# Kernel optimization log

Measured on AMD Instinct MI355X. Metric: run time of the kernel, lower is better.

The kernel has to match this reference:

```python
import jax, jax.numpy as jnp
import numpy as np

B, T, C = 4, 2048, 1024
NH, HS = 16, 64            # n_head, head_size
BL, SL = 32, 16            # block_length, stride_length


def setup_inputs() -> dict:
    key = jax.random.key(0)
    ks = jax.random.split(key, 7)
    def lin(k, shape, fan_in):
        return jax.random.normal(k, shape, jnp.float32) * (1.0 / np.sqrt(fan_in))
    return {
        "x": jax.random.normal(ks[0], (B, T, C), jnp.float32),
        "W_attn": lin(ks[1], (3 * C, C), C),          # c_attn weight (bias=False)
        "W_proj": lin(ks[2], (C, C), C),              # c_proj weight
        "pos_emb": jax.random.normal(ks[3], (T, HS), jnp.float32) * 0.02,
        "W_fc": lin(ks[4], (4 * HS, BL * HS), BL * HS),   # compression c_fc
        "W_cproj": lin(ks[5], (HS, 4 * HS), 4 * HS),      # compression c_proj
        "ln_w": jnp.ones((HS,), jnp.float32),             # compression LayerNorm (bias=False)
    }


def _compress(h, pos_emb, W_fc, W_cproj, ln_w):
    # h: [B, nh, T, hs] -> [B, nh, num_blocks, hs] ; sliding windows of len BL, stride SL
    Bb, nh, Tt, hs = h.shape
    nb = max(1, (Tt - BL) // SL + 1)
    idx = jnp.arange(nb)[:, None] * SL + jnp.arange(BL)[None, :]        # [nb, BL]
    blocks = h[:, :, idx, :] + pos_emb[:BL][None, None, None, :, :]     # [B,nh,nb,BL,hs]
    flat = blocks.reshape(Bb, nh, nb, BL * hs)
    z = jax.nn.gelu(jnp.einsum('bnkf,gf->bnkg', flat, W_fc), approximate=False)
    z = jnp.einsum('bnkg,hg->bnkh', z, W_cproj)
    mu = jnp.mean(z, axis=-1, keepdims=True)
    var = jnp.var(z, axis=-1, keepdims=True)
    return (z - mu) / jnp.sqrt(var + 1e-5) * ln_w


def reference(x, W_attn, W_proj, pos_emb, W_fc, W_cproj, ln_w):
    Bb, Tt, Cc = x.shape
    qkv = x @ W_attn.T                                   # [B,T,3C]
    q, k, v = jnp.split(qkv, 3, axis=-1)
    q = q.reshape(Bb, Tt, NH, HS).transpose(0, 2, 1, 3)  # [B,nh,T,hs]
    k = k.reshape(Bb, Tt, NH, HS).transpose(0, 2, 1, 3)
    v = v.reshape(Bb, Tt, NH, HS).transpose(0, 2, 1, 3)

    # Computed (and discarded) exactly as in the torch forward.
    _kc = _compress(k, pos_emb, W_fc, W_cproj, ln_w)
    _vc = _compress(v, pos_emb, W_fc, W_cproj, ln_w)

    # Flash branch: is_causal=True -> attn_mask=None -> plain causal SDPA
    scale = 1.0 / np.sqrt(HS)
    scores = jnp.einsum('bhqd,bhkd->bhqk', q, k) * scale          # [B,nh,T,T]
    causal = jnp.tril(jnp.ones((Tt, Tt), dtype=bool))
    scores = jnp.where(causal, scores, -jnp.inf)
    att = jax.nn.softmax(scores, axis=-1)
    y = jnp.einsum('bhqk,bhkd->bhqd', att, v)                     # [B,nh,T,hs]
    y = y.transpose(0, 2, 1, 3).reshape(Bb, Tt, Cc)
    return y @ W_proj.T
```

## Files before the change

### kernel.cpp

```cpp
#include <hip/hip_runtime.h>
#include <hip/hip_bf16.h>
#include <stdint.h>


typedef __bf16 bf16x8 __attribute__((ext_vector_type(8)));
typedef float f32x4 __attribute__((ext_vector_type(4)));
typedef __hip_bfloat16 bf16;

#define B_ 4
#define T_ 2048
#define C_ 1024
#define NH_ 16
#define HS_ 64
#define NEG_BIG (-30000.0f)
#define SCALE_LOG2E 0.180336880111f

__device__ __forceinline__ bool detect_fp32(const unsigned short* px) {
  const int lane = threadIdx.x & 63;
  const unsigned short u = px[2 * lane];
  const int e = (u >> 7) & 0xff;
  const bool plausible = (e >= 117) && (e <= 137);
  return __popcll(__ballot(plausible)) < 32;
}

__device__ __forceinline__ void load_lds16(const bf16* g, bf16* l) {
  __builtin_amdgcn_global_load_lds(
      (const __attribute__((address_space(1))) void*)(uintptr_t)g,
      (__attribute__((address_space(3))) void*)(uintptr_t)l, 16, 0, 0);
}

__device__ __forceinline__ uint4 ld8f(const void* base, size_t elt) {
  const float* fp = (const float*)base + elt;
  float4 f0 = *(const float4*)(fp);
  float4 f1 = *(const float4*)(fp + 4);
  union { bf16 h[8]; uint4 u; } r;
  r.h[0] = __float2bfloat16(f0.x); r.h[1] = __float2bfloat16(f0.y);
  r.h[2] = __float2bfloat16(f0.z); r.h[3] = __float2bfloat16(f0.w);
  r.h[4] = __float2bfloat16(f1.x); r.h[5] = __float2bfloat16(f1.y);
  r.h[6] = __float2bfloat16(f1.z); r.h[7] = __float2bfloat16(f1.w);
  return r.u;
}

__global__ __launch_bounds__(256) void convert3(
    const void* __restrict__ x, const void* __restrict__ wa,
    const void* __restrict__ wp, bf16* __restrict__ xb, bf16* __restrict__ wab,
    bf16* __restrict__ wpb, const unsigned short* __restrict__ probe) {
  const bool f32 = detect_fp32(probe);
  int blk = blockIdx.x;
  const void* src;
  bf16* dst;
  if (blk < 4096) {
    src = x; dst = xb;
  } else if (blk < 4096 + 1536) {
    blk -= 4096; src = wa; dst = wab;
  } else {
    blk -= 4096 + 1536; src = wp; dst = wpb;
  }
  const size_t i = ((size_t)blk * 256 + threadIdx.x) * 8;
  if (f32)
    *(uint4*)(dst + i) = ld8f(src, i);
  else
    *(uint4*)(dst + i) = *(const uint4*)((const bf16*)src + i);
}

template <int IN_MODE, int OUT_MODE>
__global__ __launch_bounds__(256, 2) void gemm_bt(
    const void* __restrict__ A, const void* __restrict__ B, void* __restrict__ C,
    bf16* __restrict__ k_ws, bf16* __restrict__ v_ws,
    const unsigned short* __restrict__ in_probe,
    const unsigned short* __restrict__ out_probe, int M, int N, int K) {
  __shared__ bf16 As[128 * 32];
  __shared__ bf16 Bs[128 * 32];

  const bool f32b = in_probe ? detect_fp32(in_probe) : false;
  const bool f32a = (IN_MODE == 0) && f32b;
  const bool f32out =
      (OUT_MODE == 0) && (out_probe ? detect_fp32(out_probe) : false);

  const int tid = threadIdx.x;
  const int lane = tid & 63;
  const int wid = tid >> 6;
  const int quad = lane >> 4;
  const int col = lane & 15;
  const int m0 = blockIdx.y * 128;
  const int n0 = blockIdx.x * 128;
  const int wm = (wid >> 1) * 64;
  const int wn = (wid & 1) * 64;
  const bool vsec = (OUT_MODE == 1) && ((n0 >> 10) == 2);

  const size_t arow = (size_t)(m0 + (tid >> 2));
  const size_t brow = (size_t)(n0 + (tid >> 2));
  const int chunk = (tid & 3) * 8;

  f32x4 acc[4][4] = {};

  for (int k0 = 0; k0 < K; k0 += 32) {
    const bf16* ap0;
    const bf16* ap1;
    if (IN_MODE == 0) {
      ap0 = (const bf16*)A + arow * K + chunk + k0;
      ap1 = (const bf16*)A + (arow + 64) * K + chunk + k0;
    } else {
      const int b = m0 >> 11;
      const int tloc = (m0 & 2047) + (tid >> 2);
      const size_t aoff = ((((size_t)b * NH_) + (k0 >> 6)) * T_ + tloc) * HS_ +
                          (k0 & 32) + chunk;
      ap0 = (const bf16*)A + aoff;
      ap1 = (const bf16*)A + aoff + (size_t)64 * HS_;
    }

    uint4 a0, a1, b0, b1;
    if (f32a) {
      a0 = ld8f(A, arow * K + chunk + k0);
      a1 = ld8f(A, (arow + 64) * K + chunk + k0);
    }
    if (f32b) {
      b0 = ld8f(B, brow * K + chunk + k0);
      b1 = ld8f(B, (brow + 64) * K + chunk + k0);
    }

    __syncthreads();
    if (f32a) {
      *(uint4*)(As + tid * 8) = a0;
      *(uint4*)(As + 2048 + tid * 8) = a1;
    } else {
      load_lds16(ap0, As + tid * 8);
      load_lds16(ap1, As + 2048 + tid * 8);
    }
    if (f32b) {
      *(uint4*)(Bs + tid * 8) = b0;
      *(uint4*)(Bs + 2048 + tid * 8) = b1;
    } else {
      load_lds16((const bf16*)B + brow * K + chunk + k0, Bs + tid * 8);
      load_lds16((const bf16*)B + (brow + 64) * K + chunk + k0,
                 Bs + 2048 + tid * 8);
    }
    __syncthreads();

    bf16x8 af[4], bfr[4];
#pragma unroll
    for (int t = 0; t < 4; ++t) {
      af[t] = *(const bf16x8*)(As + (wm + t * 16 + col) * 32 + quad * 8);
      bfr[t] = *(const bf16x8*)(Bs + (wn + t * 16 + col) * 32 + quad * 8);
    }
    if (vsec) {
#pragma unroll
      for (int tm = 0; tm < 4; ++tm)
#pragma unroll
        for (int tn = 0; tn < 4; ++tn)
          acc[tm][tn] = __builtin_amdgcn_mfma_f32_16x16x32_bf16(
              bfr[tn], af[tm], acc[tm][tn], 0, 0, 0);
    } else {
#pragma unroll
      for (int tm = 0; tm < 4; ++tm)
#pragma unroll
        for (int tn = 0; tn < 4; ++tn)
          acc[tm][tn] = __builtin_amdgcn_mfma_f32_16x16x32_bf16(
              af[tm], bfr[tn], acc[tm][tn], 0, 0, 0);
    }
  }

  if (OUT_MODE == 0) {
#pragma unroll
    for (int tm = 0; tm < 4; ++tm) {
      const int mrow = m0 + wm + tm * 16 + quad * 4;
#pragma unroll
      for (int tn = 0; tn < 4; ++tn) {
        const int ncol = n0 + wn + tn * 16 + col;
#pragma unroll
        for (int r = 0; r < 4; ++r) {
          if (f32out)
            ((float*)C)[(size_t)(mrow + r) * N + ncol] = acc[tm][tn][r];
          else
            ((bf16*)C)[(size_t)(mrow + r) * N + ncol] =
                __float2bfloat16(acc[tm][tn][r]);
        }
      }
    }
  } else if (vsec) {
    const int b = m0 >> 11;
#pragma unroll
    for (int tm = 0; tm < 4; ++tm) {
      const int tloc = (m0 & 2047) + wm + tm * 16 + col;
#pragma unroll
      for (int tn = 0; tn < 4; ++tn) {
        const int vch = (n0 & (C_ - 1)) + wn + tn * 16 + quad * 4;
#pragma unroll
        for (int r = 0; r < 4; ++r) {
          const int h = (vch + r) >> 6, d = (vch + r) & 63;
          v_ws[(((size_t)b * NH_ + h) * HS_ + d) * T_ + tloc] =
              __float2bfloat16(acc[tm][tn][r]);
        }
      }
    }
  } else {
    const int sect = n0 >> 10;
    bf16* dst = (sect == 0) ? (bf16*)C : k_ws;
#pragma unroll
    for (int tm = 0; tm < 4; ++tm) {
      const int mrow = m0 + wm + tm * 16 + quad * 4;
#pragma unroll
      for (int tn = 0; tn < 4; ++tn) {
        const int c = (n0 + wn + tn * 16 + col) & (C_ - 1);
        const int h = c >> 6, d = c & 63;
#pragma unroll
        for (int r = 0; r < 4; ++r) {
          const int t = (mrow + r) & (T_ - 1);
          const int b = (mrow + r) >> 11;
          dst[(((size_t)b * NH_ + h) * T_ + t) * HS_ + d] =
              __float2bfloat16(acc[tm][tn][r]);
        }
      }
    }
  }
}

template <int SPLIT>
__global__ __launch_bounds__(256, 2) void attn(
    bf16* qy, const bf16* __restrict__ kws, const bf16* __restrict__ vws,
    float* __restrict__ po, float* __restrict__ pl) {
  __shared__ bf16 Ks[64 * 72];
  __shared__ bf16 Vs[64 * 72];
  __shared__ bf16 Ps[4][32 * 72];

  const int tid = threadIdx.x;
  const int lane = tid & 63;
  const int w = tid >> 6;
  const int quad = lane >> 4;
  const int col = lane & 15;
  const int x = (int)blockIdx.x;

  int qb, ck;
  if (SPLIT) {
    const unsigned long long lo = 0xC4D5E6F7FEDCBA98ULL;
    const unsigned int hi = 0xB3A29180u;
    const unsigned int cmask = 0x00AAAA00u;
    qb = (x < 16) ? (int)((lo >> (4 * x)) & 15)
                  : (int)((hi >> (4 * (x - 16))) & 15);
    ck = (int)((cmask >> x) & 1);
  } else {
    const int gx = (int)gridDim.x;
    const int hx = gx >> 1;
    qb = (x < hx) ? (gx - 1 - x) : (x - hx);
    ck = 0;
  }

  const int bh = blockIdx.y;
  const size_t head_off = (size_t)bh * T_ * HS_;

  const int ntall = 2 * (qb + 1);
  const int kt0 = SPLIT ? ck * 16 : 0;
  const int ntiles = SPLIT ? min(ntall - kt0, 16) : ntall;

  const int qrow = qb * 128 + w * 32 + col;
  const bf16* qp = qy + head_off + (size_t)qrow * HS_ + quad * 8;
  bf16x8 qf0a = *(const bf16x8*)(qp);
  bf16x8 qf1a = *(const bf16x8*)(qp + 32);
  bf16x8 qf0b = *(const bf16x8*)(qp + 16 * HS_);
  bf16x8 qf1b = *(const bf16x8*)(qp + 16 * HS_ + 32);
#pragma unroll
  for (int j = 0; j < 8; ++j) {
    qf0a[j] = (__bf16)((float)qf0a[j] * SCALE_LOG2E);
    qf1a[j] = (__bf16)((float)qf1a[j] * SCALE_LOG2E);
    qf0b[j] = (__bf16)((float)qf0b[j] * SCALE_LOG2E);
    qf1b[j] = (__bf16)((float)qf1b[j] * SCALE_LOG2E);
  }

  bf16x8 onesf;
#pragma unroll
  for (int j = 0; j < 8; ++j) onesf[j] = (__bf16)1.0f;

  f32x4 oa[4] = {}, ob[4] = {};
  f32x4 lacca = {}, laccb = {};

  bf16* pw = &Ps[w][0];

  const int srow = tid >> 3, sch = tid & 7;
  const bf16* kg = kws + head_off + (size_t)(kt0 * 64 + srow) * HS_ + sch * 8;
  const bf16* vg = vws + ((size_t)bh * HS_ + srow) * T_ + kt0 * 64 + sch * 8;
  bf16* kl0 = Ks + srow * 72 + sch * 8;
  bf16* kl1 = Ks + (srow + 32) * 72 + sch * 8;
  bf16* vl0 = Vs + srow * 72 + sch * 8;
  bf16* vl1 = Vs + (srow + 32) * 72 + sch * 8;

  uint4 kr0 = *(const uint4*)(kg);
  uint4 kr1 = *(const uint4*)(kg + (size_t)32 * HS_);
  uint4 vr0 = *(const uint4*)(vg);
  uint4 vr1 = *(const uint4*)(vg + (size_t)32 * T_);

  const int qga = qb * 128 + w * 32 + col;
  const int diag_start = 2 * qb;

  for (int kt = 0; kt < ntiles; ++kt) {
    const int ktg = kt0 + kt;
    const int k0 = ktg * 64;
    __syncthreads();
    *(uint4*)kl0 = kr0;
    *(uint4*)kl1 = kr1;
    *(uint4*)vl0 = vr0;
    *(uint4*)vl1 = vr1;
    __syncthreads();
    if (kt + 1 < ntiles) {
      kg += (size_t)64 * HS_;
      vg += 64;
      kr0 = *(const uint4*)(kg);
      kr1 = *(const uint4*)(kg + (size_t)32 * HS_);
      vr0 = *(const uint4*)(vg);
      vr1 = *(const uint4*)(vg + (size_t)32 * T_);
    }

    f32x4 sa[4], sb[4];
#pragma unroll
    for (int nt = 0; nt < 4; ++nt) {
      const bf16* kp = Ks + (nt * 16 + col) * 72 + quad * 8;
      bf16x8 kf0 = *(const bf16x8*)(kp);
      bf16x8 kf1 = *(const bf16x8*)(kp + 32);
      f32x4 a = {-32.0f, -32.0f, -32.0f, -32.0f};
      a = __builtin_amdgcn_mfma_f32_16x16x32_bf16(kf0, qf0a, a, 0, 0, 0);
      a = __builtin_amdgcn_mfma_f32_16x16x32_bf16(kf1, qf1a, a, 0, 0, 0);
      sa[nt] = a;
      f32x4 b = {-32.0f, -32.0f, -32.0f, -32.0f};
      b = __builtin_amdgcn_mfma_f32_16x16x32_bf16(kf0, qf0b, b, 0, 0, 0);
      b = __builtin_amdgcn_mfma_f32_16x16x32_bf16(kf1, qf1b, b, 0, 0, 0);
      sb[nt] = b;
    }

    if (ktg >= diag_start) {
#pragma unroll
      for (int nt = 0; nt < 4; ++nt) {
        const int key = k0 + nt * 16 + quad * 4;
#pragma unroll
        for (int r = 0; r < 4; ++r) {
          if (key + r > qga) sa[nt][r] = NEG_BIG;
          if (key + r > qga + 16) sb[nt][r] = NEG_BIG;
        }
      }
    }

#pragma unroll
    for (int nt = 0; nt < 4; ++nt) {
      union { ushort u[4]; uint2 v; } pa, pb;
#pragma unroll
      for (int r = 0; r < 4; ++r) {
        pa.u[r] = __bfloat16_as_ushort(__float2bfloat16(exp2f(sa[nt][r])));
        pb.u[r] = __bfloat16_as_ushort(__float2bfloat16(exp2f(sb[nt][r])));
      }
      *(uint2*)(pw + col * 72 + nt * 16 + quad * 4) = pa.v;
      *(uint2*)(pw + (col + 16) * 72 + nt * 16 + quad * 4) = pb.v;
    }

    __asm__ __volatile__("s_waitcnt lgkmcnt(0)" ::: "memory");

#pragma unroll
    for (int half = 0; half < 2; ++half) {
      bf16x8 pfa = *(const bf16x8*)(pw + col * 72 + half * 32 + quad * 8);
      bf16x8 pfb = *(const bf16x8*)(pw + (col + 16) * 72 + half * 32 + quad * 8);
      lacca = __builtin_amdgcn_mfma_f32_16x16x32_bf16(pfa, onesf, lacca, 0, 0, 0);
      laccb = __builtin_amdgcn_mfma_f32_16x16x32_bf16(pfb, onesf, laccb, 0, 0, 0);
#pragma unroll
      for (int dt = 0; dt < 4; ++dt) {
        bf16x8 vf = *(const bf16x8*)(Vs + (dt * 16 + col) * 72 + half * 32 +
                                     quad * 8);
        oa[dt] = __builtin_amdgcn_mfma_f32_16x16x32_bf16(pfa, vf, oa[dt], 0, 0, 0);
        ob[dt] = __builtin_amdgcn_mfma_f32_16x16x32_bf16(pfb, vf, ob[dt], 0, 0, 0);
      }
    }
  }

  const bool dosplit = SPLIT && (qb >= 8);
  if (!dosplit) {
    float inva[4], invb[4];
#pragma unroll
    for (int r = 0; r < 4; ++r) {
      inva[r] = 1.0f / lacca[r];
      invb[r] = 1.0f / laccb[r];
    }
#pragma unroll
    for (int dt = 0; dt < 4; ++dt)
#pragma unroll
      for (int r = 0; r < 4; ++r) {
        const int qa = qb * 128 + w * 32 + quad * 4 + r;
        qy[head_off + (size_t)qa * HS_ + dt * 16 + col] =
            __float2bfloat16(oa[dt][r] * inva[r]);
        qy[head_off + (size_t)(qa + 16) * HS_ + dt * 16 + col] =
            __float2bfloat16(ob[dt][r] * invb[r]);
      }
  } else {
    const int slot = ((qb - 8) * 64 + bh) * 2 + ck;
    float* o = po + (size_t)slot * (128 * 64);
#pragma unroll
    for (int dt = 0; dt < 4; ++dt)
#pragma unroll
      for (int r = 0; r < 4; ++r) {
        const int qa = w * 32 + quad * 4 + r;
        o[(size_t)qa * 64 + dt * 16 + col] = oa[dt][r];
        o[(size_t)(qa + 16) * 64 + dt * 16 + col] = ob[dt][r];
      }
    if (col == 0) {
      float* lp = pl + (size_t)slot * 128;
#pragma unroll
      for (int r = 0; r < 4; ++r) {
        lp[w * 32 + quad * 4 + r] = lacca[r];
        lp[w * 32 + 16 + quad * 4 + r] = laccb[r];
      }
    }
  }
}

__global__ __launch_bounds__(256) void attn_combine(
    bf16* __restrict__ qy, const float* __restrict__ po,
    const float* __restrict__ pl) {
  const int qb = 8 + (int)blockIdx.x;
  const int bh = (int)blockIdx.y;
  const int pair = ((qb - 8) * 64 + bh) * 2;
  const float* o0 = po + (size_t)pair * (128 * 64);
  const float* o1 = o0 + 128 * 64;
  const float* l0 = pl + (size_t)pair * 128;
  const float* l1 = l0 + 128;
  const int q = threadIdx.x >> 1;
  const int d0 = (threadIdx.x & 1) * 32;
  const float inv = 1.0f / (l0[q] + l1[q]);
  const size_t base =
      (size_t)bh * T_ * HS_ + (size_t)(qb * 128 + q) * HS_ + d0;
  const size_t ob = (size_t)q * 64 + d0;
#pragma unroll
  for (int j0 = 0; j0 < 32; j0 += 8) {
    union { bf16 h[8]; uint4 u; } out;
#pragma unroll
    for (int j = 0; j < 8; ++j)
      out.h[j] = __float2bfloat16((o0[ob + j0 + j] + o1[ob + j0 + j]) * inv);
    *(uint4*)(qy + base + j0) = out.u;
  }
}

extern "C" void kernel_launch(void* const* d_in, const int* in_sizes, int n_in,
                              void* d_out, int out_size, void* d_ws, size_t ws_size,
                              hipStream_t stream) {
  const void* x = d_in[0];
  const void* W_attn = d_in[1];
  const void* W_proj = d_in[2];
  const unsigned short* probe = (const unsigned short*)d_in[0];

  const size_t qkv_elems = (size_t)B_ * NH_ * T_ * HS_;
  const size_t xe = (size_t)B_ * T_ * C_;
  const size_t wae = (size_t)3 * C_ * C_;
  const size_t wpe = (size_t)C_ * C_;

  bf16* q_ws = (bf16*)d_ws;
  bf16* k_ws = q_ws + qkv_elems;
  bf16* v_ws = k_ws + qkv_elems;
  bf16* x_bf = v_ws + qkv_elems;
  bf16* wa_bf = x_bf + xe;
  bf16* wp_bf = wa_bf + wae;
  const size_t need = (3 * qkv_elems + xe + wae + wpe) * sizeof(bf16);

  float* po = (float*)(wp_bf + wpe);
  float* pl = po + (size_t)1024 * 128 * 64;
  const size_t need2 =
      need + ((size_t)1024 * 128 * 64 + (size_t)1024 * 128) * sizeof(float);

  const int M = B_ * T_;

  if (ws_size >= need) {
    convert3<<<6144, 256, 0, stream>>>(x, W_attn, W_proj, x_bf, wa_bf, wp_bf,
                                       probe);
    gemm_bt<0, 1><<<dim3(3 * C_ / 128, M / 128), 256, 0, stream>>>(
        x_bf, wa_bf, q_ws, k_ws, v_ws, nullptr, nullptr, M, 3 * C_, C_);
    if (ws_size >= need2) {
      attn<1><<<dim3(24, B_ * NH_), 256, 0, stream>>>(q_ws, k_ws, v_ws, po, pl);
      attn_combine<<<dim3(8, B_ * NH_), 256, 0, stream>>>(q_ws, po, pl);
    } else {
      attn<0><<<dim3(T_ / 128, B_ * NH_), 256, 0, stream>>>(q_ws, k_ws, v_ws,
                                                            nullptr, nullptr);
    }
    gemm_bt<1, 0><<<dim3(C_ / 128, M / 128), 256, 0, stream>>>(
        q_ws, wp_bf, d_out, nullptr, nullptr, nullptr, probe, M, C_, C_);
  } else {
    gemm_bt<0, 1><<<dim3(3 * C_ / 128, M / 128), 256, 0, stream>>>(
        x, W_attn, q_ws, k_ws, v_ws, probe, nullptr, M, 3 * C_, C_);
    attn<0><<<dim3(T_ / 128, B_ * NH_), 256, 0, stream>>>(q_ws, k_ws, v_ws,
                                                          nullptr, nullptr);
    gemm_bt<1, 0><<<dim3(C_ / 128, M / 128), 256, 0, stream>>>(
        q_ws, W_proj, d_out, nullptr, nullptr, probe, probe, M, C_, C_);
  }
}
```

Before: 300.3 us.

## Double-buffer LDS tiles in GEMM to overlap global loads with MFMA

Converts the shared-memory A/B tiles in the bf16 GEMM kernel into ping-pong buffers. The next k-tile is prefetched, either by direct global-to-LDS loads or via registers for fp32 inputs, while MFMAs run on the current tile. This drops one __syncthreads per iteration and hides global load latency. LDS use doubles to 32KB per block, which with launch bounds of 2 blocks per SM is still fine, but may raise register pressure on the fp32 path.

```diff
diff --git a/kernel.cpp b/kernel.cpp
--- a/kernel.cpp
+++ b/kernel.cpp
@@ -69,8 +69,8 @@
     bf16* __restrict__ k_ws, bf16* __restrict__ v_ws,
     const unsigned short* __restrict__ in_probe,
     const unsigned short* __restrict__ out_probe, int M, int N, int K) {
-  __shared__ bf16 As[128 * 32];
-  __shared__ bf16 Bs[128 * 32];
+  __shared__ bf16 As[2][128 * 32];
+  __shared__ bf16 Bs[2][128 * 32];
 
   const bool f32b = in_probe ? detect_fp32(in_probe) : false;
   const bool f32a = (IN_MODE == 0) && f32b;
@@ -91,57 +91,76 @@
   const size_t arow = (size_t)(m0 + (tid >> 2));
   const size_t brow = (size_t)(n0 + (tid >> 2));
   const int chunk = (tid & 3) * 8;
+  const size_t astep = (IN_MODE == 0) ? (size_t)64 * K : (size_t)64 * HS_;
 
   f32x4 acc[4][4] = {};
 
+  auto a_ptr = [&](int k0) -> const bf16* {
+    if (IN_MODE == 0) return (const bf16*)A + arow * K + chunk + k0;
+    const int b = m0 >> 11;
+    const int tloc = (m0 & 2047) + (tid >> 2);
+    return (const bf16*)A +
+           ((((size_t)b * NH_) + (k0 >> 6)) * T_ + tloc) * HS_ + (k0 & 32) +
+           chunk;
+  };
+
+  if (f32a) {
+    uint4 a0 = ld8f(A, arow * K + chunk);
+    uint4 a1 = ld8f(A, (arow + 64) * K + chunk);
+    *(uint4*)(&As[0][0] + tid * 8) = a0;
+    *(uint4*)(&As[0][0] + 2048 + tid * 8) = a1;
+  } else {
+    const bf16* ap = a_ptr(0);
+    load_lds16(ap, &As[0][0] + tid * 8);
+    load_lds16(ap + astep, &As[0][0] + 2048 + tid * 8);
+  }
+  if (f32b) {
+    uint4 b0 = ld8f(B, brow * K + chunk);
+    uint4 b1 = ld8f(B, (brow + 64) * K + chunk);
+    *(uint4*)(&Bs[0][0] + tid * 8) = b0;
+    *(uint4*)(&Bs[0][0] + 2048 + tid * 8) = b1;
+  } else {
+    load_lds16((const bf16*)B + brow * K + chunk, &Bs[0][0] + tid * 8);
+    load_lds16((const bf16*)B + (brow + 64) * K + chunk,
+               &Bs[0][0] + 2048 + tid * 8);
+  }
+  __syncthreads();
+
+  int cur = 0;
   for (int k0 = 0; k0 < K; k0 += 32) {
-    const bf16* ap0;
-    const bf16* ap1;
-    if (IN_MODE == 0) {
-      ap0 = (const bf16*)A + arow * K + chunk + k0;
-      ap1 = (const bf16*)A + (arow + 64) * K + chunk + k0;
-    } else {
-      const int b = m0 >> 11;
-      const int tloc = (m0 & 2047) + (tid >> 2);
-      const size_t aoff = ((((size_t)b * NH_) + (k0 >> 6)) * T_ + tloc) * HS_ +
-                          (k0 & 32) + chunk;
-      ap0 = (const bf16*)A + aoff;
-      ap1 = (const bf16*)A + aoff + (size_t)64 * HS_;
-    }
+    const int kn = k0 + 32;
+    const bool hasn = kn < K;
+    const int nxt = cur ^ 1;
 
     uint4 a0, a1, b0, b1;
-    if (f32a) {
-      a0 = ld8f(A, arow * K + chunk + k0);
-      a1 = ld8f(A, (arow + 64) * K + chunk + k0);
-    }
-    if (f32b) {
-      b0 = ld8f(B, brow * K + chunk + k0);
-      b1 = ld8f(B, (brow + 64) * K + chunk + k0);
-    }
-
-    __syncthreads();
-    if (f32a) {
-      *(uint4*)(As + tid * 8) = a0;
-      *(uint4*)(As + 2048 + tid * 8) = a1;
-    } else {
-      load_lds16(ap0, As + tid * 8);
-      load_lds16(ap1, As + 2048 + tid * 8);
-    }
-    if (f32b) {
-      *(uint4*)(Bs + tid * 8) = b0;
-      *(uint4*)(Bs + 2048 + tid * 8) = b1;
-    } else {
-      load_lds16((const bf16*)B + brow * K + chunk + k0, Bs + tid * 8);
-      load_lds16((const bf16*)B + (brow + 64) * K + chunk + k0,
-                 Bs + 2048 + tid * 8);
-    }
-    __syncthreads();
+    bool wra = false, wrb = false;
+    if (hasn) {
+      if (f32a) {
+        a0 = ld8f(A, arow * K + chunk + kn);
+        a1 = ld8f(A, (arow + 64) * K + chunk + kn);
+        wra = true;
+      } else {
+        const bf16* ap = a_ptr(kn);
+        load_lds16(ap, &As[nxt][0] + tid * 8);
+        load_lds16(ap + astep, &As[nxt][0] + 2048 + tid * 8);
+      }
+      if (f32b) {
+        b0 = ld8f(B, brow * K + chunk + kn);
+        b1 = ld8f(B, (brow + 64) * K + chunk + kn);
+        wrb = true;
+      } else {
+        load_lds16((const bf16*)B + brow * K + chunk + kn,
+                   &Bs[nxt][0] + tid * 8);
+        load_lds16((const bf16*)B + (brow + 64) * K + chunk + kn,
+                   &Bs[nxt][0] + 2048 + tid * 8);
+      }
+    }
 
     bf16x8 af[4], bfr[4];
 #pragma unroll
     for (int t = 0; t < 4; ++t) {
-      af[t] = *(const bf16x8*)(As + (wm + t * 16 + col) * 32 + quad * 8);
-      bfr[t] = *(const bf16x8*)(Bs + (wn + t * 16 + col) * 32 + quad * 8);
+      af[t] = *(const bf16x8*)(&As[cur][0] + (wm + t * 16 + col) * 32 + quad * 8);
+      bfr[t] = *(const bf16x8*)(&Bs[cur][0] + (wn + t * 16 + col) * 32 + quad * 8);
     }
     if (vsec) {
 #pragma unroll
@@ -158,6 +177,17 @@
           acc[tm][tn] = __builtin_amdgcn_mfma_f32_16x16x32_bf16(
               af[tm], bfr[tn], acc[tm][tn], 0, 0, 0);
     }
+
+    if (wra) {
+      *(uint4*)(&As[nxt][0] + tid * 8) = a0;
+      *(uint4*)(&As[nxt][0] + 2048 + tid * 8) = a1;
+    }
+    if (wrb) {
+      *(uint4*)(&Bs[nxt][0] + tid * 8) = b0;
+      *(uint4*)(&Bs[nxt][0] + 2048 + tid * 8) = b1;
+    }
+    __syncthreads();
+    cur = nxt;
   }
 
   if (OUT_MODE == 0) {
```

Measured after the change: 285.2 us. -5.0%, faster.
